# Performance work log

Measured on AMD Instinct MI355X. Metric: run time of the kernel, lower is better.

The kernel has to match this reference:

```python
import jax, jax.numpy as jnp
import numpy as np

N = 100000
E = 1600000
IN_C = 128
HID = 32
HEADS = 4
OUT_C = 16
G = 128
NEG_SLOPE = 0.2


def setup_inputs() -> dict:
    key = jax.random.key(0)
    ks = jax.random.split(key, 16)
    x = jax.random.normal(ks[0], (N, IN_C), dtype=jnp.float32)
    edge_index = jax.random.randint(ks[1], (2, E), 0, N, dtype=jnp.int64)
    batch = jnp.sort(jax.random.randint(ks[2], (N,), 0, G, dtype=jnp.int64))
    node_weights = jax.random.uniform(ks[3], (N, 1), dtype=jnp.float32)
    s = 1.0 / np.sqrt(IN_C)
    W1 = jax.random.uniform(ks[4], (IN_C, HEADS * HID), jnp.float32, -s, s)
    att_src1 = jax.random.uniform(ks[5], (HEADS, HID), jnp.float32, -s, s)
    att_dst1 = jax.random.uniform(ks[6], (HEADS, HID), jnp.float32, -s, s)
    b1 = jnp.zeros((HEADS * HID,), jnp.float32)
    s2 = 1.0 / np.sqrt(HEADS * HID)
    W2 = jax.random.uniform(ks[7], (HEADS * HID, HID), jnp.float32, -s2, s2)
    att_src2 = jax.random.uniform(ks[8], (1, HID), jnp.float32, -s2, s2)
    att_dst2 = jax.random.uniform(ks[9], (1, HID), jnp.float32, -s2, s2)
    b2 = jnp.zeros((HID,), jnp.float32)
    s3 = 1.0 / np.sqrt(HID)
    fcW = jax.random.uniform(ks[10], (HID, OUT_C), jnp.float32, -s3, s3)
    fcb = jax.random.uniform(ks[11], (OUT_C,), jnp.float32, -s3, s3)
    return {"x": x, "edge_index": edge_index, "batch": batch,
            "node_weights": node_weights,
            "W1": W1, "att_src1": att_src1, "att_dst1": att_dst1, "b1": b1,
            "W2": W2, "att_src2": att_src2, "att_dst2": att_dst2, "b2": b2,
            "fcW": fcW, "fcb": fcb}


def gat_conv(x, src, dst, W, att_src, att_dst, bias, heads, ch, concat):
    n = x.shape[0]
    h = (x @ W).reshape(n, heads, ch)                       # [N,H,C]
    a_src = jnp.sum(h * att_src[None], axis=-1)             # [N,H]
    a_dst = jnp.sum(h * att_dst[None], axis=-1)             # [N,H]
    e = jax.nn.leaky_relu(a_src[src] + a_dst[dst], NEG_SLOPE)  # [E,H]
    # segment softmax over incoming edges of each destination node
    e_max = jax.ops.segment_max(e, dst, num_segments=n)
    ex = jnp.exp(e - e_max[dst])
    denom = jax.ops.segment_sum(ex, dst, num_segments=n)
    alpha = ex / denom[dst]                                 # [E,H]
    msg = h[src] * alpha[..., None]                         # [E,H,C]
    out = jax.ops.segment_sum(msg, dst, num_segments=n)     # [N,H,C]
    if concat:
        out = out.reshape(n, heads * ch)
    else:
        out = out.mean(axis=1)
    return out + bias


def reference(x, edge_index, batch, node_weights,
              W1, att_src1, att_dst1, b1,
              W2, att_src2, att_dst2, b2,
              fcW, fcb):
    n = x.shape[0]
    # PyG GATConv adds self-loops by default
    loop = jnp.arange(n, dtype=edge_index.dtype)
    src = jnp.concatenate([edge_index[0], loop])
    dst = jnp.concatenate([edge_index[1], loop])

    h = x * node_weights
    h = jax.nn.elu(gat_conv(h, src, dst, W1, att_src1, att_dst1, b1, HEADS, HID, True))
    h = jax.nn.elu(gat_conv(h, src, dst, W2, att_src2, att_dst2, b2, 1, HID, False))
    # global mean pool over graphs
    sums = jax.ops.segment_sum(h, batch, num_segments=G)
    cnts = jax.ops.segment_sum(jnp.ones((n,), h.dtype), batch, num_segments=G)
    pooled = sums / jnp.maximum(cnts, 1.0)[:, None]
    return pooled @ fcW + fcb
```

## Files before the change

### kernel.cpp

```cpp
#include <hip/hip_runtime.h>
#include <cstdint>

#define NGRAPH 128
#define NEG 0.2f
#define NB_MAX 512
#define BSH 8
#define BSZ 256
#define CAP 8192

typedef unsigned int uint;
typedef unsigned short ushort;
typedef unsigned char uchar;
typedef __attribute__((ext_vector_type(8))) short bf16x8;
typedef __attribute__((ext_vector_type(4))) float f32x4;
typedef __attribute__((ext_vector_type(2))) float f32x2;

union U4B { uint4 u; bf16x8 v; };

__device__ __forceinline__ ushort f2bf(float f) {
  uint u = __float_as_uint(f);
  uint r = (u + 0x7FFF + ((u >> 16) & 1)) >> 16;
  return (ushort)r;
}

__device__ __forceinline__ uint cvtpkbf16(float lo, float hi) {
  uint r;
  asm("v_cvt_pk_bf16_f32 %0, %1, %2" : "=v"(r) : "v"(lo), "v"(hi));
  return r;
}

__device__ __forceinline__ void pkfma(f32x2& acc, f32x2 f, f32x2 w) {
  asm("v_pk_fma_f32 %0, %1, %2, %0" : "+v"(acc) : "v"(f), "v"(w));
}

__device__ __forceinline__ float bperm_f(int addr, float v) {
  return __int_as_float(__builtin_amdgcn_ds_bpermute(addr, __float_as_int(v)));
}
__device__ __forceinline__ int bperm_i(int addr, int v) {
  return __builtin_amdgcn_ds_bpermute(addr, v);
}

__device__ __forceinline__ int wave_incl_scan_i(int v) {
  int lane = threadIdx.x & 63;
#pragma unroll
  for (int off = 1; off < 64; off <<= 1) {
    int u = __shfl_up(v, off, 64);
    if (lane >= off) v += u;
  }
  return v;
}

__global__ void k_bin(const int* __restrict__ ei,
                      const float* __restrict__ W1, const float* __restrict__ W2,
                      ushort* __restrict__ Wt1, ushort* __restrict__ Wt2,
                      int E, int Etot, int NB, int nbin,
                      int* __restrict__ bcur, uint* __restrict__ bbuf) {
  if (blockIdx.x >= (uint)nbin) {
    int t2 = (blockIdx.x - nbin) * 256 + threadIdx.x;
    if (t2 < 16384) {
      int n = t2 >> 7, k = t2 & 127;
      Wt1[t2] = f2bf(W1[k * 128 + n]);
    } else {
      int u = t2 - 16384;
      int n = u >> 7, k = u & 127;
      Wt2[u] = f2bf(W2[k * 32 + n]);
    }
    return;
  }
  __shared__ int h[NB_MAX];
  __shared__ int baseo[NB_MAX];
  int t = threadIdx.x;
  for (int b = t; b < NB; b += 256) h[b] = 0;
  __syncthreads();
  int cbase = blockIdx.x * 4096;
  int cend = min(cbase + 4096, Etot);
  for (int e = cbase + t; e < cend; e += 256) {
    int d = (e < E) ? ei[E + e] : (e - E);
    atomicAdd(&h[d >> BSH], 1);
  }
  __syncthreads();
  for (int b = t; b < NB; b += 256) {
    int c = h[b];
    baseo[b] = c ? atomicAdd(&bcur[b], c) : 0;
    h[b] = 0;
  }
  __syncthreads();
  for (int e = cbase + t; e < cend; e += 256) {
    int s, d;
    if (e < E) { s = ei[e]; d = ei[E + e]; } else { s = e - E; d = s; }
    int b = d >> BSH;
    int r = atomicAdd(&h[b], 1);
    bbuf[(size_t)b * CAP + baseo[b] + r] = ((uint)(d & (BSZ - 1)) << 17) | (uint)s;
  }
}

__global__ void k_bg(const uint* __restrict__ bbuf, const int* __restrict__ bcur,
                     int NB, int N, int* __restrict__ offs, int* __restrict__ ssrc,
                     const float* __restrict__ x, const ushort* __restrict__ Wt,
                     const float* __restrict__ nw, const float* __restrict__ att_s,
                     const float* __restrict__ att_d, uchar* __restrict__ hb1,
                     float* __restrict__ asrc, float* __restrict__ adst) {
  __shared__ int sst[NB_MAX + 1];
  __shared__ int wsum2[4];
  __shared__ int deg[BSZ];
  if (blockIdx.x < (uint)NB) {
    int t = threadIdx.x, lane = t & 63, wid = t >> 6;
    int v0 = (2 * t < NB) ? bcur[2 * t] : 0;
    int v1 = (2 * t + 1 < NB) ? bcur[2 * t + 1] : 0;
    int s = v0 + v1;
    int sv = wave_incl_scan_i(s);
    if (lane == 63) wsum2[wid] = sv;
    deg[t] = 0;
    __syncthreads();
    if (t == 0) {
      int r = 0;
#pragma unroll
      for (int k = 0; k < 4; k++) { int x2 = wsum2[k]; wsum2[k] = r; r += x2; }
    }
    __syncthreads();
    int excl = wsum2[wid] + sv - s;
    sst[2 * t] = excl;
    sst[2 * t + 1] = excl + v0;
    if (t == 255) sst[512] = excl + v0 + v1;
    __syncthreads();
    int b = blockIdx.x;
    int ebeg = sst[b], eend = sst[b + 1];
    int cnt = eend - ebeg;
    for (int i = t; i < cnt; i += BSZ)
      atomicAdd(&deg[bbuf[(size_t)b * CAP + i] >> 17], 1);
    __syncthreads();
    int v = deg[t];
    int sv2 = wave_incl_scan_i(v);
    if (lane == 63) wsum2[wid] = sv2;
    __syncthreads();
    if (t == 0) {
      int r = 0;
#pragma unroll
      for (int k = 0; k < 4; k++) { int x2 = wsum2[k]; wsum2[k] = r; r += x2; }
    }
    __syncthreads();
    int excl2 = wsum2[wid] + sv2 - v;
    int node = (b << BSH) + t;
    if (node < N) offs[node] = ebeg + excl2;
    if (b == 0 && t == 0) offs[N] = sst[512];
    __syncthreads();
    deg[t] = excl2;
    __syncthreads();
    for (int i = t; i < cnt; i += BSZ) {
      uint rec = bbuf[(size_t)b * CAP + i];
      int r = atomicAdd(&deg[rec >> 17], 1);
      ssrc[ebeg + r] = (int)(rec & 0x1FFFF);
    }
    return;
  }
  int bid = blockIdx.x - NB;
  int wv = threadIdx.x >> 6, l = threadIdx.x & 63;
  int lg = l >> 4, lr = l & 15;
  int row0 = bid * 64 + wv * 16;
  int node = row0 + lr;
  bool valid = node < N;
  float sc = valid ? nw[node] : 0.f;
  bf16x8 xfr[4];
  const float* xr = x + (size_t)node * 128;
#pragma unroll
  for (int kc = 0; kc < 4; kc++) {
    float v[8];
    if (valid) {
      float4 q0 = *reinterpret_cast<const float4*>(xr + kc * 32 + lg * 8);
      float4 q1 = *reinterpret_cast<const float4*>(xr + kc * 32 + lg * 8 + 4);
      v[0] = q0.x; v[1] = q0.y; v[2] = q0.z; v[3] = q0.w;
      v[4] = q1.x; v[5] = q1.y; v[6] = q1.z; v[7] = q1.w;
    } else {
#pragma unroll
      for (int j = 0; j < 8; j++) v[j] = 0.f;
    }
    U4B a;
    a.u.x = cvtpkbf16(v[0] * sc, v[1] * sc);
    a.u.y = cvtpkbf16(v[2] * sc, v[3] * sc);
    a.u.z = cvtpkbf16(v[4] * sc, v[5] * sc);
    a.u.w = cvtpkbf16(v[6] * sc, v[7] * sc);
    xfr[kc] = a.v;
  }
  float pS[4] = {}, pD[4] = {};
#pragma unroll
  for (int ct = 0; ct < 8; ct++) {
    f32x4 acc = {0.f, 0.f, 0.f, 0.f};
    const ushort* wrow = Wt + (size_t)(ct * 16 + lr) * 128;
#pragma unroll
    for (int kc = 0; kc < 4; kc++) {
      U4B bfr;
      bfr.u = *reinterpret_cast<const uint4*>(wrow + kc * 32 + lg * 8);
      acc = __builtin_amdgcn_mfma_f32_16x16x32_bf16(bfr.v, xfr[kc], acc, 0, 0, 0);
    }
    int c0 = ct * 16 + lg * 4;
    if (valid) {
      uint u8 = (uint)__builtin_amdgcn_cvt_pk_fp8_f32(acc[0], acc[1], 0, false);
      u8 = (uint)__builtin_amdgcn_cvt_pk_fp8_f32(acc[2], acc[3], u8, true);
      *reinterpret_cast<uint*>(hb1 + (size_t)node * 128 + c0) = u8;
    }
    float4 as4 = *reinterpret_cast<const float4*>(att_s + c0);
    float4 ad4 = *reinterpret_cast<const float4*>(att_d + c0);
    int h = ct >> 1;
    pS[h] += acc[0] * as4.x + acc[1] * as4.y + acc[2] * as4.z + acc[3] * as4.w;
    pD[h] += acc[0] * ad4.x + acc[1] * ad4.y + acc[2] * ad4.z + acc[3] * ad4.w;
  }
#pragma unroll
  for (int off = 16; off < 64; off <<= 1) {
#pragma unroll
    for (int h = 0; h < 4; h++) {
      pS[h] += __shfl_xor(pS[h], off, 64);
      pD[h] += __shfl_xor(pD[h], off, 64);
    }
  }
  if (lg == 0 && valid) {
    *reinterpret_cast<float4*>(asrc + node * 4) = make_float4(pS[0], pS[1], pS[2], pS[3]);
    *reinterpret_cast<float4*>(adst + node * 4) = make_float4(pD[0], pD[1], pD[2], pD[3]);
  }
}

__global__ void k_aggr1(const int* __restrict__ offs, const int* __restrict__ ssrc,
                        const uchar* __restrict__ hb, const float* __restrict__ asrc,
                        const float* __restrict__ adst, const float* __restrict__ bias,
                        const ushort* __restrict__ Wt2, const float* __restrict__ as2,
                        const float* __restrict__ ad2, uchar* __restrict__ hb2,
                        float* __restrict__ asrc2, float* __restrict__ adst2, int N) {
  __shared__ ushort rowl[4][136];
  int tid = threadIdx.x;
  int wv = tid >> 6, l = tid & 63;
  int d = blockIdx.x * 4 + wv;
  int dc = min(d, N - 1);
  int slot = l >> 3;
  int cb = l & 7;
  int h = cb >> 1;
  int hq = l & 3;
  int eidx = l >> 2;
  float adq = adst[dc * 4 + hq];
  int beg = offs[dc], end = offs[dc + 1];
  int endm1 = end - 1;
  const uchar* hbc = hb + cb * 16;
  int bp0 = (slot * 4 + h) << 2;
  int bp1 = bp0 + 128;
  f32x2 a2[8] = {};
  float dsp = 0.f;
  auto ACC = [&](uint4 p, float w) {
    f32x2 wp = {w, w};
    f32x2 f;
    f = __builtin_amdgcn_cvt_pk_f32_fp8(p.x, false); pkfma(a2[0], f, wp);
    f = __builtin_amdgcn_cvt_pk_f32_fp8(p.x, true);  pkfma(a2[1], f, wp);
    f = __builtin_amdgcn_cvt_pk_f32_fp8(p.y, false); pkfma(a2[2], f, wp);
    f = __builtin_amdgcn_cvt_pk_f32_fp8(p.y, true);  pkfma(a2[3], f, wp);
    f = __builtin_amdgcn_cvt_pk_f32_fp8(p.z, false); pkfma(a2[4], f, wp);
    f = __builtin_amdgcn_cvt_pk_f32_fp8(p.z, true);  pkfma(a2[5], f, wp);
    f = __builtin_amdgcn_cvt_pk_f32_fp8(p.w, false); pkfma(a2[6], f, wp);
    f = __builtin_amdgcn_cvt_pk_f32_fp8(p.w, true);  pkfma(a2[7], f, wp);
  };
  for (int base = beg; base < end; base += 32) {
    int eA = base + eidx;
    int eB = eA + 16;
    int sA = ssrc[min(eA, endm1)];
    int sB = ssrc[min(eB, endm1)];
    int s0 = bperm_i(bp0, sA);
    int s1 = bperm_i(bp1, sA);
    int s2 = bperm_i(bp0, sB);
    int s3 = bperm_i(bp1, sB);
    int rem = end - base;
    uint4 p0, p1, p2, p3;
    p0 = *reinterpret_cast<const uint4*>(hbc + (size_t)s0 * 128);
    if (rem > 8)  p1 = *reinterpret_cast<const uint4*>(hbc + (size_t)s1 * 128);
    if (rem > 16) p2 = *reinterpret_cast<const uint4*>(hbc + (size_t)s2 * 128);
    if (rem > 24) p3 = *reinterpret_cast<const uint4*>(hbc + (size_t)s3 * 128);
    float aA = asrc[sA * 4 + hq] + adq;
    float aB = asrc[sB * 4 + hq] + adq;
    aA = fmaxf(aA, aA * NEG);
    aB = fmaxf(aB, aB * NEG);
    float wA = (eA < end) ? __expf(aA) : 0.f;
    float wB = (eB < end) ? __expf(aB) : 0.f;
    dsp += wA + wB;
    float w0 = bperm_f(bp0, wA);
    float w1 = bperm_f(bp1, wA);
    float w2 = bperm_f(bp0, wB);
    float w3 = bperm_f(bp1, wB);
    ACC(p0, w0);
    if (rem > 8)  ACC(p1, w1);
    if (rem > 16) ACC(p2, w2);
    if (rem > 24) ACC(p3, w3);
  }
  dsp += __shfl_xor(dsp, 4, 64);
  dsp += __shfl_xor(dsp, 8, 64);
  dsp += __shfl_xor(dsp, 16, 64);
  dsp += __shfl_xor(dsp, 32, 64);
  float ds = bperm_f(h << 2, dsp);
  int b3 = (l >> 3) & 1, b4 = (l >> 4) & 1, b5 = (l >> 5) & 1;
  float t8[8];
#pragma unroll
  for (int r = 0; r < 8; r++) {
    float av = a2[r >> 1][r & 1];
    float bv = a2[(r + 8) >> 1][r & 1];
    float send = b3 ? av : bv;
    float recv = __shfl_xor(send, 8, 64);
    t8[r] = (b3 ? bv : av) + recv;
  }
  float t4[4];
#pragma unroll
  for (int r = 0; r < 4; r++) {
    float send = b4 ? t8[r] : t8[r + 4];
    float recv = __shfl_xor(send, 16, 64);
    t4[r] = (b4 ? t8[r + 4] : t8[r]) + recv;
  }
  float t2[2];
#pragma unroll
  for (int r = 0; r < 2; r++) {
    float send = b5 ? t4[r] : t4[r + 2];
    float recv = __shfl_xor(send, 32, 64);
    t2[r] = (b5 ? t4[r + 2] : t4[r]) + recv;
  }
  float inv = __builtin_amdgcn_rcpf(ds > 0.f ? ds : 1.f);
  int c0 = cb * 16 + b3 * 8 + b4 * 4 + b5 * 2;
  float2 bi = *reinterpret_cast<const float2*>(bias + c0);
  float r0 = fmaf(t2[0], inv, bi.x);
  float r1 = fmaf(t2[1], inv, bi.y);
  r0 = r0 > 0.f ? r0 : __expf(r0) - 1.f;
  r1 = r1 > 0.f ? r1 : __expf(r1) - 1.f;
  *reinterpret_cast<uint*>(&rowl[wv][c0]) = cvtpkbf16(r0, r1);
  __syncthreads();
  if (wv != 0) return;
  int lg = l >> 4, lr = l & 15;
  int rsel = lr & 3;
  bf16x8 bfrag[4];
#pragma unroll
  for (int kc = 0; kc < 4; kc++) {
    U4B bb;
    bb.u = *reinterpret_cast<const uint4*>(&rowl[rsel][kc * 32 + lg * 8]);
    bfrag[kc] = bb.v;
  }
  int dd = blockIdx.x * 4 + lr;
  bool vs = (lr < 4) && (dd < N);
  float pS = 0.f, pD = 0.f;
#pragma unroll
  for (int ct = 0; ct < 2; ct++) {
    f32x4 acc = {0.f, 0.f, 0.f, 0.f};
    const ushort* wrow = Wt2 + (size_t)(ct * 16 + lr) * 128;
#pragma unroll
    for (int kc = 0; kc < 4; kc++) {
      U4B bfr;
      bfr.u = *reinterpret_cast<const uint4*>(wrow + kc * 32 + lg * 8);
      acc = __builtin_amdgcn_mfma_f32_16x16x32_bf16(bfr.v, bfrag[kc], acc, 0, 0, 0);
    }
    int cg = ct * 16 + lg * 4;
    if (vs) {
      uint u8 = (uint)__builtin_amdgcn_cvt_pk_fp8_f32(acc[0], acc[1], 0, false);
      u8 = (uint)__builtin_amdgcn_cvt_pk_fp8_f32(acc[2], acc[3], u8, true);
      *reinterpret_cast<uint*>(hb2 + (size_t)dd * 32 + cg) = u8;
    }
    float4 as4 = *reinterpret_cast<const float4*>(as2 + cg);
    float4 ad4 = *reinterpret_cast<const float4*>(ad2 + cg);
    pS += acc[0] * as4.x + acc[1] * as4.y + acc[2] * as4.z + acc[3] * as4.w;
    pD += acc[0] * ad4.x + acc[1] * ad4.y + acc[2] * ad4.z + acc[3] * ad4.w;
  }
  pS += __shfl_xor(pS, 16, 64);
  pS += __shfl_xor(pS, 32, 64);
  pD += __shfl_xor(pD, 16, 64);
  pD += __shfl_xor(pD, 32, 64);
  if (vs && lg == 0) { asrc2[dd] = pS; adst2[dd] = pD; }
}

__global__ void k_aggr2(const int* __restrict__ offs, const int* __restrict__ ssrc,
                        const uchar* __restrict__ hb, const float* __restrict__ asrc,
                        const float* __restrict__ adst, const float* __restrict__ bias,
                        float* __restrict__ out, int N) {
  int wid = threadIdx.x >> 6, l = threadIdx.x & 63;
  int d = blockIdx.x * 4 + wid;
  if (d >= N) return;
  int slot = l >> 2;
  int k = l & 3;
  float ad = adst[d];
  int beg = offs[d], end = offs[d + 1];
  int endm1 = end - 1;
  const uchar* hbc = hb + k * 8;
  int bq0 = slot << 2;
  int bq1 = (slot + 16) << 2;
  int bq2 = (slot + 32) << 2;
  int bq3 = (slot + 48) << 2;
  f32x2 a2[4] = {};
  float dsp = 0.f;
  auto ACC2 = [&](uint2 p, float w) {
    f32x2 wp = {w, w};
    f32x2 f;
    f = __builtin_amdgcn_cvt_pk_f32_fp8(p.x, false); pkfma(a2[0], f, wp);
    f = __builtin_amdgcn_cvt_pk_f32_fp8(p.x, true);  pkfma(a2[1], f, wp);
    f = __builtin_amdgcn_cvt_pk_f32_fp8(p.y, false); pkfma(a2[2], f, wp);
    f = __builtin_amdgcn_cvt_pk_f32_fp8(p.y, true);  pkfma(a2[3], f, wp);
  };
  for (int base = beg; base < end; base += 64) {
    int e = base + l;
    int sL = ssrc[min(e, endm1)];
    int s0 = bperm_i(bq0, sL);
    int s1 = bperm_i(bq1, sL);
    int s2 = bperm_i(bq2, sL);
    int s3 = bperm_i(bq3, sL);
    int rem = end - base;
    uint2 p0, p1, p2, p3;
    p0 = *reinterpret_cast<const uint2*>(hbc + (size_t)s0 * 32);
    if (rem > 16) p1 = *reinterpret_cast<const uint2*>(hbc + (size_t)s1 * 32);
    if (rem > 32) p2 = *reinterpret_cast<const uint2*>(hbc + (size_t)s2 * 32);
    if (rem > 48) p3 = *reinterpret_cast<const uint2*>(hbc + (size_t)s3 * 32);
    float xv = asrc[sL] + ad;
    xv = fmaxf(xv, xv * NEG);
    float wL = (e < end) ? __expf(xv) : 0.f;
    dsp += wL;
    float w0 = bperm_f(bq0, wL);
    float w1 = bperm_f(bq1, wL);
    float w2 = bperm_f(bq2, wL);
    float w3 = bperm_f(bq3, wL);
    ACC2(p0, w0);
    if (rem > 16) ACC2(p1, w1);
    if (rem > 32) ACC2(p2, w2);
    if (rem > 48) ACC2(p3, w3);
  }
  dsp += __shfl_xor(dsp, 1, 64);
  dsp += __shfl_xor(dsp, 2, 64);
  dsp += __shfl_xor(dsp, 4, 64);
  dsp += __shfl_xor(dsp, 8, 64);
  dsp += __shfl_xor(dsp, 16, 64);
  dsp += __shfl_xor(dsp, 32, 64);
  int b2 = (l >> 2) & 1, b3 = (l >> 3) & 1, b4 = (l >> 4) & 1;
  float t4[4];
#pragma unroll
  for (int r = 0; r < 4; r++) {
    float av = a2[r >> 1][r & 1];
    float bv = a2[(r + 4) >> 1][r & 1];
    float send = b2 ? av : bv;
    float recv = __shfl_xor(send, 4, 64);
    t4[r] = (b2 ? bv : av) + recv;
  }
  float t2[2];
#pragma unroll
  for (int r = 0; r < 2; r++) {
    float send = b3 ? t4[r] : t4[r + 2];
    float recv = __shfl_xor(send, 8, 64);
    t2[r] = (b3 ? t4[r + 2] : t4[r]) + recv;
  }
  float send = b4 ? t2[0] : t2[1];
  float recv = __shfl_xor(send, 16, 64);
  float t1 = (b4 ? t2[1] : t2[0]) + recv;
  t1 += __shfl_xor(t1, 32, 64);
  if (l < 32) {
    int c = k * 8 + b2 * 4 + b3 * 2 + b4;
    float inv = __builtin_amdgcn_rcpf(dsp > 0.f ? dsp : 1.f);
    float r = fmaf(t1, inv, bias[c]);
    r = r > 0.f ? r : __expf(r) - 1.f;
    out[(size_t)d * 32 + c] = r;
  }
}

__global__ void k_pool_fc(const float* __restrict__ h2, const int* __restrict__ batch,
                          const float* __restrict__ fcW, const float* __restrict__ fcb,
                          float* __restrict__ out, int N) {
  int g = blockIdx.x;
  int lo = 0, hi = N;
  while (lo < hi) { int mid = (lo + hi) >> 1; if (batch[mid] < g) lo = mid + 1; else hi = mid; }
  int beg = lo;
  hi = N;
  while (lo < hi) { int mid = (lo + hi) >> 1; if (batch[mid] < g + 1) lo = mid + 1; else hi = mid; }
  int end = lo;
  int t = threadIdx.x, c = t & 31, sub = t >> 5;
  float acc = 0.f;
  for (int n = beg + sub; n < end; n += 8) acc += h2[(size_t)n * 32 + c];
  __shared__ float red[8][32];
  __shared__ float pooled[32];
  red[sub][c] = acc;
  __syncthreads();
  if (sub == 0) {
    float s = 0.f;
#pragma unroll
    for (int i = 0; i < 8; i++) s += red[i][c];
    float cnt = (float)(end - beg);
    pooled[c] = s / fmaxf(cnt, 1.f);
  }
  __syncthreads();
  if (t < 16) {
    float r = fcb[t];
#pragma unroll
    for (int cc = 0; cc < 32; cc++) r += pooled[cc] * fcW[cc * 16 + t];
    out[g * 16 + t] = r;
  }
}

extern "C" void kernel_launch(void* const* d_in, const int* in_sizes, int n_in,
                              void* d_out, int out_size, void* d_ws, size_t ws_size,
                              hipStream_t stream) {
  const float* x     = (const float*)d_in[0];
  const int*   ei    = (const int*)d_in[1];
  const int*   batch = (const int*)d_in[2];
  const float* nw    = (const float*)d_in[3];
  const float* W1    = (const float*)d_in[4];
  const float* as1w  = (const float*)d_in[5];
  const float* ad1w  = (const float*)d_in[6];
  const float* b1    = (const float*)d_in[7];
  const float* W2    = (const float*)d_in[8];
  const float* as2w  = (const float*)d_in[9];
  const float* ad2w  = (const float*)d_in[10];
  const float* b2    = (const float*)d_in[11];
  const float* fcW   = (const float*)d_in[12];
  const float* fcb   = (const float*)d_in[13];
  float* out = (float*)d_out;

  const int N = in_sizes[0] / 128;
  const int E = in_sizes[1] / 2;
  const int Etot = E + N;
  const int NB = (N + BSZ - 1) >> BSH;

  char* w = (char*)d_ws;
  size_t ofs = 0;
  auto alloc = [&](size_t bytes) {
    char* p = w + ofs;
    ofs += (bytes + 255) & ~(size_t)255;
    return p;
  };
  uchar*  hb1    = (uchar*)alloc((size_t)N * 128);
  uchar*  hb2    = (uchar*)alloc((size_t)N * 32);
  float*  h2     = (float*)alloc((size_t)N * 32 * 4);
  float*  asrc1  = (float*)alloc((size_t)N * 4 * 4);
  float*  adst1  = (float*)alloc((size_t)N * 4 * 4);
  float*  asrc2  = (float*)alloc((size_t)N * 4);
  float*  adst2  = (float*)alloc((size_t)N * 4);
  ushort* Wt1    = (ushort*)alloc(16384 * 2);
  ushort* Wt2    = (ushort*)alloc(4096 * 2);
  int*    bcur   = (int*)alloc((size_t)NB * 4);
  int*    offs   = (int*)alloc((size_t)(N + 1) * 4);
  uint*   bbuf   = (uint*)alloc((size_t)NB * CAP * 4);
  int*    ssrc   = (int*)alloc((size_t)Etot * 4);

  hipMemsetAsync(bcur, 0, (size_t)NB * 4, stream);

  const int nbin = (Etot + 4095) / 4096;
  k_bin<<<nbin + 80, 256, 0, stream>>>(ei, W1, W2, Wt1, Wt2, E, Etot, NB, nbin, bcur, bbuf);

  const int ngemm1 = (N + 63) / 64;
  k_bg<<<NB + ngemm1, 256, 0, stream>>>(bbuf, bcur, NB, N, offs, ssrc,
                                        x, Wt1, nw, as1w, ad1w, hb1, asrc1, adst1);

  k_aggr1<<<(N + 3) / 4, 256, 0, stream>>>(offs, ssrc, hb1, asrc1, adst1, b1,
                                           Wt2, as2w, ad2w, hb2, asrc2, adst2, N);

  k_aggr2<<<(N + 3) / 4, 256, 0, stream>>>(offs, ssrc, hb2, asrc2, adst2, b2, h2, N);

  k_pool_fc<<<NGRAPH, 256, 0, stream>>>(h2, batch, fcW, fcb, out, N);
}
```

Measured before the change: 305.1 us.

## Replace two-level binned CSR build with global degree count, scan, and atomic scatter

Replaces the bucketed CSR construction (local histogram, per-bin buffer, per-bin scan and scatter) with a direct approach. Degrees are counted with global atomics, a decoupled block scan hands out offsets through a global atomic counter, and edges are scattered through per-node atomic cursors. Aggregation kernels now compute each row's end as offs plus deg. This removes the large intermediate bin buffer and its extra read pass, at the cost of more global atomics, an extra kernel launch, and worse write locality in the scatter. The atomic block-offset assignment does not follow block order, and the order of edges within each row is now nondeterministic.

```diff
diff --git a/kernel.cpp b/kernel.cpp
--- a/kernel.cpp
+++ b/kernel.cpp
@@ -3,10 +3,6 @@
 
 #define NGRAPH 128
 #define NEG 0.2f
-#define NB_MAX 512
-#define BSH 8
-#define BSZ 256
-#define CAP 8192
 
 typedef unsigned int uint;
 typedef unsigned short ushort;
@@ -50,11 +46,10 @@
   return v;
 }
 
-__global__ void k_bin(const int* __restrict__ ei,
+__global__ void k_deg(const int* __restrict__ ei,
                       const float* __restrict__ W1, const float* __restrict__ W2,
                       ushort* __restrict__ Wt1, ushort* __restrict__ Wt2,
-                      int E, int Etot, int NB, int nbin,
-                      int* __restrict__ bcur, uint* __restrict__ bbuf) {
+                      int E, int Etot, int nbin, int* __restrict__ deg) {
   if (blockIdx.x >= (uint)nbin) {
     int t2 = (blockIdx.x - nbin) * 256 + threadIdx.x;
     if (t2 < 16384) {
@@ -67,93 +62,53 @@
     }
     return;
   }
-  __shared__ int h[NB_MAX];
-  __shared__ int baseo[NB_MAX];
-  int t = threadIdx.x;
-  for (int b = t; b < NB; b += 256) h[b] = 0;
+  int idx = blockIdx.x * 256 + threadIdx.x;
+  int stride = nbin * 256;
+  for (int e = idx; e < Etot; e += stride) {
+    int d = (e < E) ? ei[E + e] : (e - E);
+    atomicAdd(&deg[d], 1);
+  }
+}
+
+__global__ void k_off(const int* __restrict__ deg, int N, int* __restrict__ gcur,
+                      int* __restrict__ offs, int* __restrict__ cursor) {
+  __shared__ int wsum[4];
+  __shared__ int sbase;
+  int t = threadIdx.x, lane = t & 63, wid = t >> 6;
+  int node = blockIdx.x * 256 + t;
+  int v = (node < N) ? deg[node] : 0;
+  int sv = wave_incl_scan_i(v);
+  if (lane == 63) wsum[wid] = sv;
   __syncthreads();
-  int cbase = blockIdx.x * 4096;
-  int cend = min(cbase + 4096, Etot);
-  for (int e = cbase + t; e < cend; e += 256) {
-    int d = (e < E) ? ei[E + e] : (e - E);
-    atomicAdd(&h[d >> BSH], 1);
+  if (t == 0) {
+    int r = 0;
+#pragma unroll
+    for (int k = 0; k < 4; k++) { int x2 = wsum[k]; wsum[k] = r; r += x2; }
+    sbase = atomicAdd(gcur, r);
   }
   __syncthreads();
-  for (int b = t; b < NB; b += 256) {
-    int c = h[b];
-    baseo[b] = c ? atomicAdd(&bcur[b], c) : 0;
-    h[b] = 0;
-  }
-  __syncthreads();
-  for (int e = cbase + t; e < cend; e += 256) {
-    int s, d;
-    if (e < E) { s = ei[e]; d = ei[E + e]; } else { s = e - E; d = s; }
-    int b = d >> BSH;
-    int r = atomicAdd(&h[b], 1);
-    bbuf[(size_t)b * CAP + baseo[b] + r] = ((uint)(d & (BSZ - 1)) << 17) | (uint)s;
-  }
-}
-
-__global__ void k_bg(const uint* __restrict__ bbuf, const int* __restrict__ bcur,
-                     int NB, int N, int* __restrict__ offs, int* __restrict__ ssrc,
-                     const float* __restrict__ x, const ushort* __restrict__ Wt,
+  int excl = sbase + wsum[wid] + sv - v;
+  if (node < N) { offs[node] = excl; cursor[node] = excl; }
+}
+
+__global__ void k_sg(const int* __restrict__ ei, int E, int Etot, int nsc,
+                     int* __restrict__ cursor, int* __restrict__ ssrc,
+                     int N, const float* __restrict__ x, const ushort* __restrict__ Wt,
                      const float* __restrict__ nw, const float* __restrict__ att_s,
                      const float* __restrict__ att_d, uchar* __restrict__ hb1,
                      float* __restrict__ asrc, float* __restrict__ adst) {
-  __shared__ int sst[NB_MAX + 1];
-  __shared__ int wsum2[4];
-  __shared__ int deg[BSZ];
-  if (blockIdx.x < (uint)NB) {
-    int t = threadIdx.x, lane = t & 63, wid = t >> 6;
-    int v0 = (2 * t < NB) ? bcur[2 * t] : 0;
-    int v1 = (2 * t + 1 < NB) ? bcur[2 * t + 1] : 0;
-    int s = v0 + v1;
-    int sv = wave_incl_scan_i(s);
-    if (lane == 63) wsum2[wid] = sv;
-    deg[t] = 0;
-    __syncthreads();
-    if (t == 0) {
-      int r = 0;
-#pragma unroll
-      for (int k = 0; k < 4; k++) { int x2 = wsum2[k]; wsum2[k] = r; r += x2; }
-    }
-    __syncthreads();
-    int excl = wsum2[wid] + sv - s;
-    sst[2 * t] = excl;
-    sst[2 * t + 1] = excl + v0;
-    if (t == 255) sst[512] = excl + v0 + v1;
-    __syncthreads();
-    int b = blockIdx.x;
-    int ebeg = sst[b], eend = sst[b + 1];
-    int cnt = eend - ebeg;
-    for (int i = t; i < cnt; i += BSZ)
-      atomicAdd(&deg[bbuf[(size_t)b * CAP + i] >> 17], 1);
-    __syncthreads();
-    int v = deg[t];
-    int sv2 = wave_incl_scan_i(v);
-    if (lane == 63) wsum2[wid] = sv2;
-    __syncthreads();
-    if (t == 0) {
-      int r = 0;
-#pragma unroll
-      for (int k = 0; k < 4; k++) { int x2 = wsum2[k]; wsum2[k] = r; r += x2; }
-    }
-    __syncthreads();
-    int excl2 = wsum2[wid] + sv2 - v;
-    int node = (b << BSH) + t;
-    if (node < N) offs[node] = ebeg + excl2;
-    if (b == 0 && t == 0) offs[N] = sst[512];
-    __syncthreads();
-    deg[t] = excl2;
-    __syncthreads();
-    for (int i = t; i < cnt; i += BSZ) {
-      uint rec = bbuf[(size_t)b * CAP + i];
-      int r = atomicAdd(&deg[rec >> 17], 1);
-      ssrc[ebeg + r] = (int)(rec & 0x1FFFF);
+  if (blockIdx.x < (uint)nsc) {
+    int idx = blockIdx.x * 256 + threadIdx.x;
+    int stride = nsc * 256;
+    for (int e = idx; e < Etot; e += stride) {
+      int s, d;
+      if (e < E) { s = ei[e]; d = ei[E + e]; } else { s = e - E; d = s; }
+      int pos = atomicAdd(&cursor[d], 1);
+      ssrc[pos] = s;
     }
     return;
   }
-  int bid = blockIdx.x - NB;
+  int bid = blockIdx.x - nsc;
   int wv = threadIdx.x >> 6, l = threadIdx.x & 63;
   int lg = l >> 4, lr = l & 15;
   int row0 = bid * 64 + wv * 16;
@@ -218,7 +173,8 @@
   }
 }
 
-__global__ void k_aggr1(const int* __restrict__ offs, const int* __restrict__ ssrc,
+__global__ void k_aggr1(const int* __restrict__ offs, const int* __restrict__ deg,
+                        const int* __restrict__ ssrc,
                         const uchar* __restrict__ hb, const float* __restrict__ asrc,
                         const float* __restrict__ adst, const float* __restrict__ bias,
                         const ushort* __restrict__ Wt2, const float* __restrict__ as2,
@@ -235,7 +191,8 @@
   int hq = l & 3;
   int eidx = l >> 2;
   float adq = adst[dc * 4 + hq];
-  int beg = offs[dc], end = offs[dc + 1];
+  int beg = offs[dc];
+  int end = beg + deg[dc];
   int endm1 = end - 1;
   const uchar* hbc = hb + cb * 16;
   int bp0 = (slot * 4 + h) << 2;
@@ -364,7 +321,8 @@
   if (vs && lg == 0) { asrc2[dd] = pS; adst2[dd] = pD; }
 }
 
-__global__ void k_aggr2(const int* __restrict__ offs, const int* __restrict__ ssrc,
+__global__ void k_aggr2(const int* __restrict__ offs, const int* __restrict__ deg,
+                        const int* __restrict__ ssrc,
                         const uchar* __restrict__ hb, const float* __restrict__ asrc,
                         const float* __restrict__ adst, const float* __restrict__ bias,
                         float* __restrict__ out, int N) {
@@ -374,7 +332,8 @@
   int slot = l >> 2;
   int k = l & 3;
   float ad = adst[d];
-  int beg = offs[d], end = offs[d + 1];
+  int beg = offs[d];
+  int end = beg + deg[d];
   int endm1 = end - 1;
   const uchar* hbc = hb + k * 8;
   int bq0 = slot << 2;
@@ -508,7 +467,7 @@
   const int N = in_sizes[0] / 128;
   const int E = in_sizes[1] / 2;
   const int Etot = E + N;
-  const int NB = (N + BSZ - 1) >> BSH;
+  const int NBK = (N + 255) >> 8;
 
   char* w = (char*)d_ws;
   size_t ofs = 0;
@@ -526,24 +485,28 @@
   float*  adst2  = (float*)alloc((size_t)N * 4);
   ushort* Wt1    = (ushort*)alloc(16384 * 2);
   ushort* Wt2    = (ushort*)alloc(4096 * 2);
-  int*    bcur   = (int*)alloc((size_t)NB * 4);
-  int*    offs   = (int*)alloc((size_t)(N + 1) * 4);
-  uint*   bbuf   = (uint*)alloc((size_t)NB * CAP * 4);
+  int*    deg    = (int*)alloc((size_t)(N + 1) * 4);
+  int*    offs   = (int*)alloc((size_t)N * 4);
+  int*    cursor = (int*)alloc((size_t)N * 4);
   int*    ssrc   = (int*)alloc((size_t)Etot * 4);
-
-  hipMemsetAsync(bcur, 0, (size_t)NB * 4, stream);
-
-  const int nbin = (Etot + 4095) / 4096;
-  k_bin<<<nbin + 80, 256, 0, stream>>>(ei, W1, W2, Wt1, Wt2, E, Etot, NB, nbin, bcur, bbuf);
-
+  int*    gcur   = deg + N;
+
+  hipMemsetAsync(deg, 0, (size_t)(N + 1) * 4, stream);
+
+  const int nbin = 1024;
+  k_deg<<<nbin + 80, 256, 0, stream>>>(ei, W1, W2, Wt1, Wt2, E, Etot, nbin, deg);
+
+  k_off<<<NBK, 256, 0, stream>>>(deg, N, gcur, offs, cursor);
+
+  const int nsc = 1024;
   const int ngemm1 = (N + 63) / 64;
-  k_bg<<<NB + ngemm1, 256, 0, stream>>>(bbuf, bcur, NB, N, offs, ssrc,
-                                        x, Wt1, nw, as1w, ad1w, hb1, asrc1, adst1);
-
-  k_aggr1<<<(N + 3) / 4, 256, 0, stream>>>(offs, ssrc, hb1, asrc1, adst1, b1,
+  k_sg<<<nsc + ngemm1, 256, 0, stream>>>(ei, E, Etot, nsc, cursor, ssrc,
+                                         N, x, Wt1, nw, as1w, ad1w, hb1, asrc1, adst1);
+
+  k_aggr1<<<(N + 3) / 4, 256, 0, stream>>>(offs, deg, ssrc, hb1, asrc1, adst1, b1,
                                            Wt2, as2w, ad2w, hb2, asrc2, adst2, N);
 
-  k_aggr2<<<(N + 3) / 4, 256, 0, stream>>>(offs, ssrc, hb2, asrc2, adst2, b2, h2, N);
+  k_aggr2<<<(N + 3) / 4, 256, 0, stream>>>(offs, deg, ssrc, hb2, asrc2, adst2, b2, h2, N);
 
   k_pool_fc<<<NGRAPH, 256, 0, stream>>>(h2, batch, fcW, fcb, out, N);
 }
```

Result: slower. 490.9 us (+60.9%).
